# Kernel optimization log

Hardware: AMD Instinct MI355X
Metric: run time of the kernel (lower is better)

The kernel has to match this reference:

```python
import jax, jax.numpy as jnp
import numpy as np

B, H, L, T, V, LAYERS = 512, 256, 256, 64, 128, 2
SOS = 0


def setup_inputs() -> dict:
    key = jax.random.key(0)
    ks = jax.random.split(key, 10)
    s = 0.05
    return {
        "x": jax.random.normal(ks[0], (B, H, 1, L), jnp.float32),          # encoder memory
        "y": jax.random.randint(ks[1], (B, T), 0, V, jnp.int32),            # teacher tokens
        "emb": jax.random.normal(ks[2], (V, H), jnp.float32) * s,           # embedding table
        "attn_w": jax.random.normal(ks[3], (L, 2 * H), jnp.float32) * s,    # attn Linear [out,in]
        "attn_b": jnp.zeros((L,), jnp.float32),
        "comb_w": jax.random.normal(ks[4], (H, 2 * H), jnp.float32) * s,    # attn_combine
        "comb_b": jnp.zeros((H,), jnp.float32),
        "gru_w_ih": jax.random.normal(ks[5], (LAYERS, 3 * H, H), jnp.float32) * s,
        "gru_w_hh": jax.random.normal(ks[6], (LAYERS, 3 * H, H), jnp.float32) * s,
        "gru_b_ih": jnp.zeros((LAYERS, 3 * H), jnp.float32),
        "gru_b_hh": jnp.zeros((LAYERS, 3 * H), jnp.float32),
        "out_w": jax.random.normal(ks[7], (V, H), jnp.float32) * s,
        "out_b": jnp.zeros((V,), jnp.float32),
    }


def reference(x, y, emb, attn_w, attn_b, comb_w, comb_b,
              gru_w_ih, gru_w_hh, gru_b_ih, gru_b_hh, out_w, out_b):
    # x: [B, H, 1, L] -> encoder memory enc: [B, L, H]
    enc = jnp.transpose(x[:, :, 0, :], (0, 2, 1))
    b = x.shape[0]
    h0 = jnp.zeros((LAYERS, b, H), x.dtype)
    # teacher forcing: input at step t is y[:, t-1], with SOS at t=0
    tokens = jnp.concatenate([jnp.full((b, 1), SOS, y.dtype), y[:, :-1]], axis=1)  # [B, T]

    def step(hidden, tok):
        e = emb[tok]  # [B, H] (dropout disabled / eval mode)
        scores = jnp.concatenate([e, hidden[0]], axis=1) @ attn_w.T + attn_b  # [B, L]
        aw = jax.nn.softmax(scores, axis=1)
        applied = jnp.einsum('bl,blh->bh', aw, enc)  # [B, H]
        g = jax.nn.relu(jnp.concatenate([applied, e], axis=1) @ comb_w.T + comb_b)
        xin = g
        hs = []
        for l in range(LAYERS):  # single-step multilayer GRU (PyTorch equations)
            gi = xin @ gru_w_ih[l].T + gru_b_ih[l]
            gh = hidden[l] @ gru_w_hh[l].T + gru_b_hh[l]
            ir, iz, inn = jnp.split(gi, 3, axis=1)
            hr, hz, hn = jnp.split(gh, 3, axis=1)
            r = jax.nn.sigmoid(ir + hr)
            z = jax.nn.sigmoid(iz + hz)
            n = jnp.tanh(inn + r * hn)
            hnew = (1 - z) * n + z * hidden[l]
            hs.append(hnew)
            xin = hnew
        logp = jax.nn.log_softmax(xin @ out_w.T + out_b, axis=1)  # [B, V]
        return jnp.stack(hs), (logp, aw)

    _, (outs, attns) = jax.lax.scan(step, h0, tokens.T)  # outs: [T,B,V], attns: [T,B,L]
    return jnp.transpose(outs, (1, 2, 0)), jnp.transpose(attns, (1, 0, 2))
```

## Files before the change

kernel.cpp:

```cpp
#include <hip/hip_runtime.h>
#include <math.h>

#define B 512
#define H 256
#define L 256
#define T 64
#define V 128
#define LAYERS 2
#define SOS 0

#define OFF_A 0
#define OFF_C 131072
#define OFF_G 262144
#define GRU_LAYER_STRIDE (6 * 65536)
#define GRU_MAT_STRIDE 65536
#define OFF_O (OFF_G + LAYERS * GRU_LAYER_STRIDE)
#define WS_HALVES (OFF_O + 32768)
#define OFF_XT WS_HALVES
#define XT_B_STRIDE (32 * 256 * 8)
#define XT_HALVES ((size_t)B * XT_B_STRIDE)
#define WS_NEED_BYTES ((size_t)(OFF_XT + XT_HALVES) * 2)

typedef _Float16 half8 __attribute__((ext_vector_type(8)));
typedef _Float16 half2t __attribute__((ext_vector_type(2)));
typedef unsigned int u32x4 __attribute__((ext_vector_type(4)));
typedef float f32x4 __attribute__((ext_vector_type(4)));

__device__ __forceinline__ float fdot2(half2t a, half2t b, float c) {
#if __has_builtin(__builtin_amdgcn_fdot2)
    return __builtin_amdgcn_fdot2(a, b, c, false);
#else
    return c + (float)a[0] * (float)b[0] + (float)a[1] * (float)b[1];
#endif
}

union H8 {
    half8 v;
    half2t p[4];
    u32x4 u;
};

__device__ __forceinline__ half8 nt_load_h8(const _Float16* p) {
    H8 t;
    t.u = __builtin_nontemporal_load((const u32x4*)p);
    return t.v;
}

__device__ __forceinline__ float sigmoidf_(float v) {
    return 1.f / (1.f + __expf(-v));
}
__device__ __forceinline__ float fast_tanh(float v) {
    v = fminf(fmaxf(v, -15.f), 15.f);
    float e = __expf(-2.f * v);
    return (1.f - e) / (1.f + e);
}

__global__ void prep_pack(const float* __restrict__ attn_w,
                          const float* __restrict__ comb_w,
                          const float* __restrict__ gru_w_ih,
                          const float* __restrict__ gru_w_hh,
                          const float* __restrict__ out_w,
                          _Float16* __restrict__ ws) {
    int stride = gridDim.x * blockDim.x;
    for (int idx = blockIdx.x * blockDim.x + threadIdx.x; idx < WS_HALVES; idx += stride) {
        float val;
        if (idx < OFF_C) {
            int i = idx & 7, r = idx >> 3;
            int l = r & 255, k8 = r >> 8;
            val = attn_w[l * 512 + k8 * 8 + i];
        } else if (idx < OFF_G) {
            int e = idx - OFF_C;
            int i = e & 7, r = e >> 3;
            int hh = r & 255, k8 = r >> 8;
            val = comb_w[hh * 512 + k8 * 8 + i];
        } else if (idx < OFF_O) {
            int e = idx - OFF_G;
            int layer = e / GRU_LAYER_STRIDE;
            e -= layer * GRU_LAYER_STRIDE;
            int mat = e >> 16;
            e &= 65535;
            int i = e & 7, r = e >> 3;
            int j = r & 255, k8 = r >> 8;
            int k = k8 * 8 + i;
            const float* src = (mat < 3) ? gru_w_ih : gru_w_hh;
            int gate = (mat < 3) ? mat : mat - 3;
            val = src[layer * (768 * 256) + (gate * 256 + j) * 256 + k];
        } else {
            int e = idx - OFF_O;
            int i = e & 7, r = e >> 3;
            int v = r & 127, k8 = r >> 7;
            val = out_w[v * 256 + k8 * 8 + i];
        }
        ws[idx] = (_Float16)val;
    }
}

__global__ void prep_x(const float* __restrict__ x, _Float16* __restrict__ xt) {
    const int b = blockIdx.x;
    const int h = threadIdx.x;
    const float* xr = x + ((size_t)b * H + h) * L;
    _Float16* base = xt + (size_t)b * XT_B_STRIDE + h * 8;
#pragma unroll 4
    for (int k8 = 0; k8 < 32; ++k8) {
        float4 v0 = *(const float4*)(xr + k8 * 8);
        float4 v1 = *(const float4*)(xr + k8 * 8 + 4);
        half8 o;
        o[0] = (_Float16)v0.x; o[1] = (_Float16)v0.y;
        o[2] = (_Float16)v0.z; o[3] = (_Float16)v0.w;
        o[4] = (_Float16)v1.x; o[5] = (_Float16)v1.y;
        o[6] = (_Float16)v1.z; o[7] = (_Float16)v1.w;
        *(half8*)(base + k8 * 2048) = o;
    }
}

template <bool USE_XT>
__global__ __launch_bounds__(512, 2) void decoder_kernel(
    const float* __restrict__ x,
    const int* __restrict__ y,
    const float* __restrict__ emb,
    const float* __restrict__ attn_b,
    const float* __restrict__ comb_b,
    const float* __restrict__ gru_b_ih,
    const float* __restrict__ gru_b_hh,
    const float* __restrict__ out_b,
    const _Float16* __restrict__ wsh,
    const _Float16* __restrict__ xt,
    float* __restrict__ out) {
    __shared__ __align__(16) _Float16 ehf[2][512];
    __shared__ __align__(16) _Float16 hfs[LAYERS][2][256];
    __shared__ __align__(16) float h32[LAYERS][2][256];
    __shared__ __align__(16) _Float16 apf[2][256];
    __shared__ __align__(16) _Float16 gfv[2][256];
    __shared__ __align__(16) _Float16 awf[2][256];
    __shared__ __align__(16) float aw32[2][256];
    __shared__ __align__(16) float pbuf[2][2][3][256];
    __shared__ __align__(16) float po[2][2][128];
    __shared__ __align__(16) float lgbuf[2][128][33];

    const int tid = threadIdx.x;
    const int G = tid >> 8;
    const int h = tid & 255;
    const int lane = tid & 63;
    const int w = tid >> 6;
    const int b0 = blockIdx.x * 2;

    const _Float16* AW = wsh + OFF_A;
    const _Float16* CW = wsh + OFF_C;
    const _Float16* OW = wsh + OFF_O;

    const float ab = attn_b[h];
    const float cb = comb_b[h];
    const float ob = (h < V) ? out_b[h] : 0.f;
    float b_ir[LAYERS], b_iz[LAYERS], b_in[LAYERS], b_hr[LAYERS], b_hz[LAYERS], b_hn[LAYERS];
#pragma unroll
    for (int l = 0; l < LAYERS; ++l) {
        b_ir[l] = gru_b_ih[l * 768 + h];
        b_iz[l] = gru_b_ih[l * 768 + 256 + h];
        b_in[l] = gru_b_ih[l * 768 + 512 + h];
        b_hr[l] = gru_b_hh[l * 768 + h];
        b_hz[l] = gru_b_hh[l * 768 + 256 + h];
        b_hn[l] = gru_b_hh[l * 768 + 512 + h];
    }

#pragma unroll
    for (int l = 0; l < LAYERS; ++l) {
        h32[l][G][h] = 0.f;
        hfs[l][G][h] = (_Float16)0.f;
    }
    ehf[G][256 + h] = (_Float16)0.f;
    __syncthreads();

    for (int t = 0; t < T; ++t) {
        {
            int tok = (t == 0) ? SOS : y[(b0 + G) * T + (t - 1)];
            ehf[G][h] = (_Float16)emb[tok * H + h];
        }
        __syncthreads();

        {
            float a00 = 0.f, a01 = 0.f, a10 = 0.f, a11 = 0.f;
            const _Float16* wp = AW + ((G * 32) << 11) + (h << 3);
            const _Float16* e0 = &ehf[0][G << 8];
            const _Float16* e1 = &ehf[1][G << 8];
#pragma unroll 4
            for (int k8 = 0; k8 < 32; ++k8) {
                H8 uw, u0, u1;
                uw.v = *(const half8*)(wp + (k8 << 11));
                u0.v = *(const half8*)(e0 + (k8 << 3));
                u1.v = *(const half8*)(e1 + (k8 << 3));
                a00 = fdot2(uw.p[0], u0.p[0], a00);
                a00 = fdot2(uw.p[1], u0.p[1], a00);
                a01 = fdot2(uw.p[2], u0.p[2], a01);
                a01 = fdot2(uw.p[3], u0.p[3], a01);
                a10 = fdot2(uw.p[0], u1.p[0], a10);
                a10 = fdot2(uw.p[1], u1.p[1], a10);
                a11 = fdot2(uw.p[2], u1.p[2], a11);
                a11 = fdot2(uw.p[3], u1.p[3], a11);
            }
            float bias = (G == 0) ? ab : 0.f;
            pbuf[G][0][0][h] = a00 + a01 + bias;
            pbuf[G][1][0][h] = a10 + a11 + bias;
        }
        __syncthreads();

        if (w < 2) {
            const int r = w;
            float s0 = pbuf[0][r][0][lane] + pbuf[1][r][0][lane];
            float s1 = pbuf[0][r][0][lane + 64] + pbuf[1][r][0][lane + 64];
            float s2 = pbuf[0][r][0][lane + 128] + pbuf[1][r][0][lane + 128];
            float s3 = pbuf[0][r][0][lane + 192] + pbuf[1][r][0][lane + 192];
            float m = fmaxf(fmaxf(s0, s1), fmaxf(s2, s3));
            for (int off = 32; off; off >>= 1) m = fmaxf(m, __shfl_xor(m, off));
            float e0 = __expf(s0 - m), e1 = __expf(s1 - m);
            float e2 = __expf(s2 - m), e3 = __expf(s3 - m);
            float s = e0 + e1 + e2 + e3;
            for (int off = 32; off; off >>= 1) s += __shfl_xor(s, off);
            float inv = 1.f / s;
            e0 *= inv; e1 *= inv; e2 *= inv; e3 *= inv;
            if (USE_XT) {
                awf[r][lane] = (_Float16)e0;
                awf[r][lane + 64] = (_Float16)e1;
                awf[r][lane + 128] = (_Float16)e2;
                awf[r][lane + 192] = (_Float16)e3;
            } else {
                aw32[r][lane] = e0;
                aw32[r][lane + 64] = e1;
                aw32[r][lane + 128] = e2;
                aw32[r][lane + 192] = e3;
            }
            float* outA = out + (size_t)B * V * T + ((size_t)(b0 + r) * T + t) * L;
            __builtin_nontemporal_store(e0, outA + lane);
            __builtin_nontemporal_store(e1, outA + lane + 64);
            __builtin_nontemporal_store(e2, outA + lane + 128);
            __builtin_nontemporal_store(e3, outA + lane + 192);
        }
        __syncthreads();

        if (USE_XT) {
            const _Float16* xrow = xt + (size_t)(b0 + G) * XT_B_STRIDE + (h << 3);
            const _Float16* ap = &awf[G][0];
            float a0 = 0.f, a1 = 0.f;
#pragma unroll 4
            for (int k8 = 0; k8 < 32; ++k8) {
                H8 uw, ua;
                uw.v = nt_load_h8(xrow + (k8 << 11));
                ua.v = *(const half8*)(ap + (k8 << 3));
                a0 = fdot2(uw.p[0], ua.p[0], a0);
                a0 = fdot2(uw.p[1], ua.p[1], a0);
                a1 = fdot2(uw.p[2], ua.p[2], a1);
                a1 = fdot2(uw.p[3], ua.p[3], a1);
            }
            apf[G][h] = (_Float16)(a0 + a1);
        } else {
            const float* xrow = x + ((size_t)(b0 + G) * H + h) * L;
            float a0 = 0.f, a1 = 0.f;
#pragma unroll 4
            for (int l = 0; l < L; l += 8) {
                float4 x0 = *(const float4*)(xrow + l);
                float4 x1 = *(const float4*)(xrow + l + 4);
                float4 w0 = *(const float4*)&aw32[G][l];
                float4 w1 = *(const float4*)&aw32[G][l + 4];
                a0 += x0.x * w0.x + x0.y * w0.y + x0.z * w0.z + x0.w * w0.w;
                a1 += x1.x * w1.x + x1.y * w1.y + x1.z * w1.z + x1.w * w1.w;
            }
            apf[G][h] = (_Float16)(a0 + a1);
        }
        __syncthreads();

        {
            float a00 = 0.f, a01 = 0.f, a10 = 0.f, a11 = 0.f;
            const _Float16* wp = CW + ((G * 32) << 11) + (h << 3);
            const _Float16* i0 = (G == 0) ? &apf[0][0] : &ehf[0][0];
            const _Float16* i1 = (G == 0) ? &apf[1][0] : &ehf[1][0];
#pragma unroll 4
            for (int k8 = 0; k8 < 32; ++k8) {
                H8 uw, u0, u1;
                uw.v = *(const half8*)(wp + (k8 << 11));
                u0.v = *(const half8*)(i0 + (k8 << 3));
                u1.v = *(const half8*)(i1 + (k8 << 3));
                a00 = fdot2(uw.p[0], u0.p[0], a00);
                a00 = fdot2(uw.p[1], u0.p[1], a00);
                a01 = fdot2(uw.p[2], u0.p[2], a01);
                a01 = fdot2(uw.p[3], u0.p[3], a01);
                a10 = fdot2(uw.p[0], u1.p[0], a10);
                a10 = fdot2(uw.p[1], u1.p[1], a10);
                a11 = fdot2(uw.p[2], u1.p[2], a11);
                a11 = fdot2(uw.p[3], u1.p[3], a11);
            }
            pbuf[G][0][1][h] = a00 + a01;
            pbuf[G][1][1][h] = a10 + a11;
        }
        __syncthreads();
        gfv[G][h] = (_Float16)fmaxf(pbuf[0][G][1][h] + pbuf[1][G][1][h] + cb, 0.f);
        __syncthreads();

#pragma unroll
        for (int layer = 0; layer < LAYERS; ++layer) {
            const _Float16* GW = wsh + OFF_G + layer * GRU_LAYER_STRIDE + G * 3 * GRU_MAT_STRIDE;
            const _Float16* act0;
            const _Float16* act1;
            if (G == 0) {
                act0 = (layer == 0) ? &gfv[0][0] : &hfs[0][0][0];
                act1 = (layer == 0) ? &gfv[1][0] : &hfs[0][1][0];
            } else {
                act0 = &hfs[layer][0][0];
                act1 = &hfs[layer][1][0];
            }
            float aA0 = 0.f, aB0 = 0.f, aC0 = 0.f, aA1 = 0.f, aB1 = 0.f, aC1 = 0.f;
#pragma unroll 4
            for (int k8 = 0; k8 < 32; ++k8) {
                H8 w0, w1, w2, u0, u1;
                const int off = (k8 << 11) + (h << 3);
                w0.v = *(const half8*)(GW + off);
                w1.v = *(const half8*)(GW + GRU_MAT_STRIDE + off);
                w2.v = *(const half8*)(GW + 2 * GRU_MAT_STRIDE + off);
                u0.v = *(const half8*)(act0 + (k8 << 3));
                u1.v = *(const half8*)(act1 + (k8 << 3));
#pragma unroll
                for (int p = 0; p < 4; ++p) {
                    aA0 = fdot2(w0.p[p], u0.p[p], aA0);
                    aB0 = fdot2(w1.p[p], u0.p[p], aB0);
                    aC0 = fdot2(w2.p[p], u0.p[p], aC0);
                    aA1 = fdot2(w0.p[p], u1.p[p], aA1);
                    aB1 = fdot2(w1.p[p], u1.p[p], aB1);
                    aC1 = fdot2(w2.p[p], u1.p[p], aC1);
                }
            }
            pbuf[G][0][0][h] = aA0;
            pbuf[G][0][1][h] = aB0;
            pbuf[G][0][2][h] = aC0;
            pbuf[G][1][0][h] = aA1;
            pbuf[G][1][1][h] = aB1;
            pbuf[G][1][2][h] = aC1;
            __syncthreads();
            {
                float gi_r = pbuf[0][G][0][h], gi_z = pbuf[0][G][1][h], gi_n = pbuf[0][G][2][h];
                float gh_r = pbuf[1][G][0][h], gh_z = pbuf[1][G][1][h], gh_n = pbuf[1][G][2][h];
                float rr = sigmoidf_(gi_r + b_ir[layer] + gh_r + b_hr[layer]);
                float zz = sigmoidf_(gi_z + b_iz[layer] + gh_z + b_hz[layer]);
                float nn = fast_tanh(gi_n + b_in[layer] + rr * (gh_n + b_hn[layer]));
                float hnew = (1.f - zz) * nn + zz * h32[layer][G][h];
                h32[layer][G][h] = hnew;
                hfs[layer][G][h] = (_Float16)hnew;
                if (layer == 0) ehf[G][256 + h] = (_Float16)hnew;
            }
            __syncthreads();
        }

        {
            const int v = h & 127;
            const int kh = h >> 7;
            const _Float16* hp = &hfs[1][G][0] + (kh << 7);
            const _Float16* wp = OW + ((kh * 16) << 10) + (v << 3);
            float a0 = 0.f, a1 = 0.f;
#pragma unroll 4
            for (int k8 = 0; k8 < 16; ++k8) {
                H8 uw, ua;
                uw.v = *(const half8*)(wp + (k8 << 10));
                ua.v = *(const half8*)(hp + (k8 << 3));
                a0 = fdot2(uw.p[0], ua.p[0], a0);
                a0 = fdot2(uw.p[1], ua.p[1], a0);
                a1 = fdot2(uw.p[2], ua.p[2], a1);
                a1 = fdot2(uw.p[3], ua.p[3], a1);
            }
            po[kh][G][v] = a0 + a1 + ((kh == 0) ? ob : 0.f);
        }
        __syncthreads();

        if (w < 2) {
            const int r = w;
            float l0 = po[0][r][lane] + po[1][r][lane];
            float l1 = po[0][r][lane + 64] + po[1][r][lane + 64];
            float m = fmaxf(l0, l1);
            for (int off = 32; off; off >>= 1) m = fmaxf(m, __shfl_xor(m, off));
            float s = __expf(l0 - m) + __expf(l1 - m);
            for (int off = 32; off; off >>= 1) s += __shfl_xor(s, off);
            float lse = m + __logf(s);
            lgbuf[r][lane][t & 31] = l0 - lse;
            lgbuf[r][lane + 64][t & 31] = l1 - lse;
        }

        if ((t & 31) == 31) {
            __syncthreads();
            const int tb = t & ~31;
#pragma unroll
            for (int c = 0; c < 4; ++c) {
                int fidx = c * 512 + tid;
                int r = fidx >> 10;
                int rem = fidx & 1023;
                int v = rem >> 3;
                int tq = (rem & 7) << 2;
                f32x4 vec = {lgbuf[r][v][tq], lgbuf[r][v][tq + 1],
                             lgbuf[r][v][tq + 2], lgbuf[r][v][tq + 3]};
                float* dst = out + (size_t)(b0 + r) * V * T + (size_t)v * T + tb + tq;
                __builtin_nontemporal_store(vec, (f32x4*)dst);
            }
        }
    }
}

extern "C" void kernel_launch(void* const* d_in, const int* in_sizes, int n_in,
                              void* d_out, int out_size, void* d_ws, size_t ws_size,
                              hipStream_t stream) {
    const float* x = (const float*)d_in[0];
    const int* y = (const int*)d_in[1];
    const float* emb = (const float*)d_in[2];
    const float* attn_w = (const float*)d_in[3];
    const float* attn_b = (const float*)d_in[4];
    const float* comb_w = (const float*)d_in[5];
    const float* comb_b = (const float*)d_in[6];
    const float* gru_w_ih = (const float*)d_in[7];
    const float* gru_w_hh = (const float*)d_in[8];
    const float* gru_b_ih = (const float*)d_in[9];
    const float* gru_b_hh = (const float*)d_in[10];
    const float* out_w = (const float*)d_in[11];
    const float* out_b = (const float*)d_in[12];
    float* out = (float*)d_out;
    _Float16* ws = (_Float16*)d_ws;

    prep_pack<<<512, 256, 0, stream>>>(attn_w, comb_w, gru_w_ih, gru_w_hh, out_w, ws);
    if (ws_size >= WS_NEED_BYTES) {
        _Float16* xt = ws + OFF_XT;
        prep_x<<<B, 256, 0, stream>>>(x, xt);
        decoder_kernel<true><<<B / 2, 512, 0, stream>>>(
            x, y, emb, attn_b, comb_b, gru_b_ih, gru_b_hh, out_b, ws, xt, out);
    } else {
        decoder_kernel<false><<<B / 2, 512, 0, stream>>>(
            x, y, emb, attn_b, comb_b, gru_b_ih, gru_b_hh, out_b, ws, nullptr, out);
    }
}
```

Before: 2.025 ms.

## Split K across four thread groups with 1024-thread decoder blocks

Doubles the block size to 1024 threads and splits every matvec (attention scores, attention apply, combine, GRU gates, output projection) along the reduction dimension across four groups. Partial sums go through shared memory and are added before each nonlinearity. This shortens each thread's serial dot-product loop to raise parallelism per batch pair, since the grid has only 256 blocks. In exchange it adds extra shared-memory reductions and barriers per step, and the elementwise phases now leave half the threads idle.

```diff
diff --git a/kernel.cpp b/kernel.cpp
--- a/kernel.cpp
+++ b/kernel.cpp
@@ -114,7 +114,7 @@
 }
 
 template <bool USE_XT>
-__global__ __launch_bounds__(512, 2) void decoder_kernel(
+__global__ __launch_bounds__(1024, 4) void decoder_kernel(
     const float* __restrict__ x,
     const int* __restrict__ y,
     const float* __restrict__ emb,
@@ -133,8 +133,9 @@
     __shared__ __align__(16) _Float16 gfv[2][256];
     __shared__ __align__(16) _Float16 awf[2][256];
     __shared__ __align__(16) float aw32[2][256];
-    __shared__ __align__(16) float pbuf[2][2][3][256];
-    __shared__ __align__(16) float po[2][2][128];
+    __shared__ __align__(16) float pbuf[4][2][256];
+    __shared__ __align__(16) float pgru[4][2][3][256];
+    __shared__ __align__(16) float po[4][2][128];
     __shared__ __align__(16) float lgbuf[2][128][33];
 
     const int tid = threadIdx.x;
@@ -150,7 +151,7 @@
 
     const float ab = attn_b[h];
     const float cb = comb_b[h];
-    const float ob = (h < V) ? out_b[h] : 0.f;
+    const float ob = out_b[h & 127];
     float b_ir[LAYERS], b_iz[LAYERS], b_in[LAYERS], b_hr[LAYERS], b_hz[LAYERS], b_hn[LAYERS];
 #pragma unroll
     for (int l = 0; l < LAYERS; ++l) {
@@ -162,16 +163,18 @@
         b_hn[l] = gru_b_hh[l * 768 + 512 + h];
     }
 
+    if (G < 2) {
 #pragma unroll
-    for (int l = 0; l < LAYERS; ++l) {
-        h32[l][G][h] = 0.f;
-        hfs[l][G][h] = (_Float16)0.f;
-    }
-    ehf[G][256 + h] = (_Float16)0.f;
+        for (int l = 0; l < LAYERS; ++l) {
+            h32[l][G][h] = 0.f;
+            hfs[l][G][h] = (_Float16)0.f;
+        }
+        ehf[G][256 + h] = (_Float16)0.f;
+    }
     __syncthreads();
 
     for (int t = 0; t < T; ++t) {
-        {
+        if (G < 2) {
             int tok = (t == 0) ? SOS : y[(b0 + G) * T + (t - 1)];
             ehf[G][h] = (_Float16)emb[tok * H + h];
         }
@@ -179,11 +182,11 @@
 
         {
             float a00 = 0.f, a01 = 0.f, a10 = 0.f, a11 = 0.f;
-            const _Float16* wp = AW + ((G * 32) << 11) + (h << 3);
-            const _Float16* e0 = &ehf[0][G << 8];
-            const _Float16* e1 = &ehf[1][G << 8];
-#pragma unroll 4
-            for (int k8 = 0; k8 < 32; ++k8) {
+            const _Float16* wp = AW + ((G * 16) << 11) + (h << 3);
+            const _Float16* e0 = &ehf[0][G << 7];
+            const _Float16* e1 = &ehf[1][G << 7];
+#pragma unroll 4
+            for (int k8 = 0; k8 < 16; ++k8) {
                 H8 uw, u0, u1;
                 uw.v = *(const half8*)(wp + (k8 << 11));
                 u0.v = *(const half8*)(e0 + (k8 << 3));
@@ -198,17 +201,17 @@
                 a11 = fdot2(uw.p[3], u1.p[3], a11);
             }
             float bias = (G == 0) ? ab : 0.f;
-            pbuf[G][0][0][h] = a00 + a01 + bias;
-            pbuf[G][1][0][h] = a10 + a11 + bias;
+            pbuf[G][0][h] = a00 + a01 + bias;
+            pbuf[G][1][h] = a10 + a11 + bias;
         }
         __syncthreads();
 
         if (w < 2) {
             const int r = w;
-            float s0 = pbuf[0][r][0][lane] + pbuf[1][r][0][lane];
-            float s1 = pbuf[0][r][0][lane + 64] + pbuf[1][r][0][lane + 64];
-            float s2 = pbuf[0][r][0][lane + 128] + pbuf[1][r][0][lane + 128];
-            float s3 = pbuf[0][r][0][lane + 192] + pbuf[1][r][0][lane + 192];
+            float s0 = pbuf[0][r][lane] + pbuf[1][r][lane] + pbuf[2][r][lane] + pbuf[3][r][lane];
+            float s1 = pbuf[0][r][lane + 64] + pbuf[1][r][lane + 64] + pbuf[2][r][lane + 64] + pbuf[3][r][lane + 64];
+            float s2 = pbuf[0][r][lane + 128] + pbuf[1][r][lane + 128] + pbuf[2][r][lane + 128] + pbuf[3][r][lane + 128];
+            float s3 = pbuf[0][r][lane + 192] + pbuf[1][r][lane + 192] + pbuf[2][r][lane + 192] + pbuf[3][r][lane + 192];
             float m = fmaxf(fmaxf(s0, s1), fmaxf(s2, s3));
             for (int off = 32; off; off >>= 1) m = fmaxf(m, __shfl_xor(m, off));
             float e0 = __expf(s0 - m), e1 = __expf(s1 - m);
@@ -236,44 +239,52 @@
         }
         __syncthreads();
 
-        if (USE_XT) {
-            const _Float16* xrow = xt + (size_t)(b0 + G) * XT_B_STRIDE + (h << 3);
-            const _Float16* ap = &awf[G][0];
-            float a0 = 0.f, a1 = 0.f;
-#pragma unroll 4
-            for (int k8 = 0; k8 < 32; ++k8) {
-                H8 uw, ua;
-                uw.v = nt_load_h8(xrow + (k8 << 11));
-                ua.v = *(const half8*)(ap + (k8 << 3));
-                a0 = fdot2(uw.p[0], ua.p[0], a0);
-                a0 = fdot2(uw.p[1], ua.p[1], a0);
-                a1 = fdot2(uw.p[2], ua.p[2], a1);
-                a1 = fdot2(uw.p[3], ua.p[3], a1);
-            }
-            apf[G][h] = (_Float16)(a0 + a1);
-        } else {
-            const float* xrow = x + ((size_t)(b0 + G) * H + h) * L;
-            float a0 = 0.f, a1 = 0.f;
-#pragma unroll 4
-            for (int l = 0; l < L; l += 8) {
-                float4 x0 = *(const float4*)(xrow + l);
-                float4 x1 = *(const float4*)(xrow + l + 4);
-                float4 w0 = *(const float4*)&aw32[G][l];
-                float4 w1 = *(const float4*)&aw32[G][l + 4];
-                a0 += x0.x * w0.x + x0.y * w0.y + x0.z * w0.z + x0.w * w0.w;
-                a1 += x1.x * w1.x + x1.y * w1.y + x1.z * w1.z + x1.w * w1.w;
-            }
-            apf[G][h] = (_Float16)(a0 + a1);
-        }
+        {
+            const int r = G & 1;
+            const int q = G >> 1;
+            if (USE_XT) {
+                const _Float16* xrow = xt + (size_t)(b0 + r) * XT_B_STRIDE + (q << 15) + (h << 3);
+                const _Float16* ap = &awf[r][q << 7];
+                float a0 = 0.f, a1 = 0.f;
+#pragma unroll 4
+                for (int k8 = 0; k8 < 16; ++k8) {
+                    H8 uw, ua;
+                    uw.v = nt_load_h8(xrow + (k8 << 11));
+                    ua.v = *(const half8*)(ap + (k8 << 3));
+                    a0 = fdot2(uw.p[0], ua.p[0], a0);
+                    a0 = fdot2(uw.p[1], ua.p[1], a0);
+                    a1 = fdot2(uw.p[2], ua.p[2], a1);
+                    a1 = fdot2(uw.p[3], ua.p[3], a1);
+                }
+                pbuf[G][0][h] = a0 + a1;
+            } else {
+                const float* xrow = x + ((size_t)(b0 + r) * H + h) * L + (q << 7);
+                const float* ap = &aw32[r][q << 7];
+                float a0 = 0.f, a1 = 0.f;
+#pragma unroll 4
+                for (int l = 0; l < 128; l += 8) {
+                    float4 x0 = *(const float4*)(xrow + l);
+                    float4 x1 = *(const float4*)(xrow + l + 4);
+                    float4 w0 = *(const float4*)(ap + l);
+                    float4 w1 = *(const float4*)(ap + l + 4);
+                    a0 += x0.x * w0.x + x0.y * w0.y + x0.z * w0.z + x0.w * w0.w;
+                    a1 += x1.x * w1.x + x1.y * w1.y + x1.z * w1.z + x1.w * w1.w;
+                }
+                pbuf[G][0][h] = a0 + a1;
+            }
+        }
+        __syncthreads();
+
+        if (G < 2) apf[G][h] = (_Float16)(pbuf[G][0][h] + pbuf[G + 2][0][h]);
         __syncthreads();
 
         {
             float a00 = 0.f, a01 = 0.f, a10 = 0.f, a11 = 0.f;
-            const _Float16* wp = CW + ((G * 32) << 11) + (h << 3);
-            const _Float16* i0 = (G == 0) ? &apf[0][0] : &ehf[0][0];
-            const _Float16* i1 = (G == 0) ? &apf[1][0] : &ehf[1][0];
-#pragma unroll 4
-            for (int k8 = 0; k8 < 32; ++k8) {
+            const _Float16* wp = CW + ((G * 16) << 11) + (h << 3);
+            const _Float16* i0 = (G < 2) ? &apf[0][G << 7] : &ehf[0][(G - 2) << 7];
+            const _Float16* i1 = (G < 2) ? &apf[1][G << 7] : &ehf[1][(G - 2) << 7];
+#pragma unroll 4
+            for (int k8 = 0; k8 < 16; ++k8) {
                 H8 uw, u0, u1;
                 uw.v = *(const half8*)(wp + (k8 << 11));
                 u0.v = *(const half8*)(i0 + (k8 << 3));
@@ -287,30 +298,35 @@
                 a11 = fdot2(uw.p[2], u1.p[2], a11);
                 a11 = fdot2(uw.p[3], u1.p[3], a11);
             }
-            pbuf[G][0][1][h] = a00 + a01;
-            pbuf[G][1][1][h] = a10 + a11;
-        }
-        __syncthreads();
-        gfv[G][h] = (_Float16)fmaxf(pbuf[0][G][1][h] + pbuf[1][G][1][h] + cb, 0.f);
+            pbuf[G][0][h] = a00 + a01;
+            pbuf[G][1][h] = a10 + a11;
+        }
+        __syncthreads();
+        if (G < 2)
+            gfv[G][h] = (_Float16)fmaxf(
+                pbuf[0][G][h] + pbuf[1][G][h] + pbuf[2][G][h] + pbuf[3][G][h] + cb, 0.f);
         __syncthreads();
 
 #pragma unroll
         for (int layer = 0; layer < LAYERS; ++layer) {
-            const _Float16* GW = wsh + OFF_G + layer * GRU_LAYER_STRIDE + G * 3 * GRU_MAT_STRIDE;
+            const int mh = G >> 1;
+            const int kq = G & 1;
+            const _Float16* GW = wsh + OFF_G + layer * GRU_LAYER_STRIDE +
+                                 mh * 3 * GRU_MAT_STRIDE + ((kq * 16) << 11) + (h << 3);
             const _Float16* act0;
             const _Float16* act1;
-            if (G == 0) {
-                act0 = (layer == 0) ? &gfv[0][0] : &hfs[0][0][0];
-                act1 = (layer == 0) ? &gfv[1][0] : &hfs[0][1][0];
+            if (mh == 0) {
+                act0 = ((layer == 0) ? &gfv[0][0] : &hfs[0][0][0]) + (kq << 7);
+                act1 = ((layer == 0) ? &gfv[1][0] : &hfs[0][1][0]) + (kq << 7);
             } else {
-                act0 = &hfs[layer][0][0];
-                act1 = &hfs[layer][1][0];
+                act0 = &hfs[layer][0][0] + (kq << 7);
+                act1 = &hfs[layer][1][0] + (kq << 7);
             }
             float aA0 = 0.f, aB0 = 0.f, aC0 = 0.f, aA1 = 0.f, aB1 = 0.f, aC1 = 0.f;
 #pragma unroll 4
-            for (int k8 = 0; k8 < 32; ++k8) {
+            for (int k8 = 0; k8 < 16; ++k8) {
                 H8 w0, w1, w2, u0, u1;
-                const int off = (k8 << 11) + (h << 3);
+                const int off = k8 << 11;
                 w0.v = *(const half8*)(GW + off);
                 w1.v = *(const half8*)(GW + GRU_MAT_STRIDE + off);
                 w2.v = *(const half8*)(GW + 2 * GRU_MAT_STRIDE + off);
@@ -326,35 +342,40 @@
                     aC1 = fdot2(w2.p[p], u1.p[p], aC1);
                 }
             }
-            pbuf[G][0][0][h] = aA0;
-            pbuf[G][0][1][h] = aB0;
-            pbuf[G][0][2][h] = aC0;
-            pbuf[G][1][0][h] = aA1;
-            pbuf[G][1][1][h] = aB1;
-            pbuf[G][1][2][h] = aC1;
+            pgru[G][0][0][h] = aA0;
+            pgru[G][0][1][h] = aB0;
+            pgru[G][0][2][h] = aC0;
+            pgru[G][1][0][h] = aA1;
+            pgru[G][1][1][h] = aB1;
+            pgru[G][1][2][h] = aC1;
             __syncthreads();
-            {
-                float gi_r = pbuf[0][G][0][h], gi_z = pbuf[0][G][1][h], gi_n = pbuf[0][G][2][h];
-                float gh_r = pbuf[1][G][0][h], gh_z = pbuf[1][G][1][h], gh_n = pbuf[1][G][2][h];
+            if (G < 2) {
+                const int r = G;
+                float gi_r = pgru[0][r][0][h] + pgru[1][r][0][h];
+                float gi_z = pgru[0][r][1][h] + pgru[1][r][1][h];
+                float gi_n = pgru[0][r][2][h] + pgru[1][r][2][h];
+                float gh_r = pgru[2][r][0][h] + pgru[3][r][0][h];
+                float gh_z = pgru[2][r][1][h] + pgru[3][r][1][h];
+                float gh_n = pgru[2][r][2][h] + pgru[3][r][2][h];
                 float rr = sigmoidf_(gi_r + b_ir[layer] + gh_r + b_hr[layer]);
                 float zz = sigmoidf_(gi_z + b_iz[layer] + gh_z + b_hz[layer]);
                 float nn = fast_tanh(gi_n + b_in[layer] + rr * (gh_n + b_hn[layer]));
-                float hnew = (1.f - zz) * nn + zz * h32[layer][G][h];
-                h32[layer][G][h] = hnew;
-                hfs[layer][G][h] = (_Float16)hnew;
-                if (layer == 0) ehf[G][256 + h] = (_Float16)hnew;
+                float hnew = (1.f - zz) * nn + zz * h32[layer][r][h];
+                h32[layer][r][h] = hnew;
+                hfs[layer][r][h] = (_Float16)hnew;
+                if (layer == 0) ehf[r][256 + h] = (_Float16)hnew;
             }
             __syncthreads();
         }
 
         {
             const int v = h & 127;
-            const int kh = h >> 7;
-            const _Float16* hp = &hfs[1][G][0] + (kh << 7);
-            const _Float16* wp = OW + ((kh * 16) << 10) + (v << 3);
+            const int r = h >> 7;
+            const _Float16* hp = &hfs[1][r][0] + (G << 6);
+            const _Float16* wp = OW + ((G * 8) << 10) + (v << 3);
             float a0 = 0.f, a1 = 0.f;
 #pragma unroll 4
-            for (int k8 = 0; k8 < 16; ++k8) {
+            for (int k8 = 0; k8 < 8; ++k8) {
                 H8 uw, ua;
                 uw.v = *(const half8*)(wp + (k8 << 10));
                 ua.v = *(const half8*)(hp + (k8 << 3));
@@ -363,14 +384,14 @@
                 a1 = fdot2(uw.p[2], ua.p[2], a1);
                 a1 = fdot2(uw.p[3], ua.p[3], a1);
             }
-            po[kh][G][v] = a0 + a1 + ((kh == 0) ? ob : 0.f);
+            po[G][r][v] = a0 + a1 + ((G == 0) ? ob : 0.f);
         }
         __syncthreads();
 
         if (w < 2) {
             const int r = w;
-            float l0 = po[0][r][lane] + po[1][r][lane];
-            float l1 = po[0][r][lane + 64] + po[1][r][lane + 64];
+            float l0 = po[0][r][lane] + po[1][r][lane] + po[2][r][lane] + po[3][r][lane];
+            float l1 = po[0][r][lane + 64] + po[1][r][lane + 64] + po[2][r][lane + 64] + po[3][r][lane + 64];
             float m = fmaxf(l0, l1);
             for (int off = 32; off; off >>= 1) m = fmaxf(m, __shfl_xor(m, off));
             float s = __expf(l0 - m) + __expf(l1 - m);
@@ -384,8 +405,8 @@
             __syncthreads();
             const int tb = t & ~31;
 #pragma unroll
-            for (int c = 0; c < 4; ++c) {
-                int fidx = c * 512 + tid;
+            for (int c = 0; c < 2; ++c) {
+                int fidx = c * 1024 + tid;
                 int r = fidx >> 10;
                 int rem = fidx & 1023;
                 int v = rem >> 3;
@@ -422,10 +443,10 @@
     if (ws_size >= WS_NEED_BYTES) {
         _Float16* xt = ws + OFF_XT;
         prep_x<<<B, 256, 0, stream>>>(x, xt);
-        decoder_kernel<true><<<B / 2, 512, 0, stream>>>(
+        decoder_kernel<true><<<B / 2, 1024, 0, stream>>>(
             x, y, emb, attn_b, comb_b, gru_b_ih, gru_b_hh, out_b, ws, xt, out);
     } else {
-        decoder_kernel<false><<<B / 2, 512, 0, stream>>>(
+        decoder_kernel<false><<<B / 2, 1024, 0, stream>>>(
             x, y, emb, attn_b, comb_b, gru_b_ih, gru_b_hh, out_b, ws, nullptr, out);
     }
 }
```

New measurement: 2.087 ms. +3.1%, slower.

## Precompute embedding projection tables and stage GRU/output weights in registers and LDS

Applied to the files above, without the earlier changes.

Adds a prep kernel that precomputes attn_w·emb and comb_w·emb per vocabulary token, so each step looks up a table entry instead of doing the embedding half of the attention and combine matmuls. This halves the K dimension of those two matmuls. It also keeps part of the GRU weights resident in registers and LDS across all timesteps and moves the output projection weights into LDS, cutting repeated global loads. The logit staging buffer is shrunk to flush every 8 steps. The costs are heavy register and LDS pressure, which may lower occupancy under launch_bounds(512,2), and the tables are rounded to fp16.

```diff
diff --git a/kernel.cpp b/kernel.cpp
--- a/kernel.cpp
+++ b/kernel.cpp
@@ -15,11 +15,16 @@
 #define GRU_LAYER_STRIDE (6 * 65536)
 #define GRU_MAT_STRIDE 65536
 #define OFF_O (OFF_G + LAYERS * GRU_LAYER_STRIDE)
-#define WS_HALVES (OFF_O + 32768)
+#define OFF_SE (OFF_O + 32768)
+#define OFF_CE (OFF_SE + 32768)
+#define WS_HALVES (OFF_CE + 32768)
 #define OFF_XT WS_HALVES
 #define XT_B_STRIDE (32 * 256 * 8)
 #define XT_HALVES ((size_t)B * XT_B_STRIDE)
 #define WS_NEED_BYTES ((size_t)(OFF_XT + XT_HALVES) * 2)
+
+#define PREG 6
+#define KLDS PREG
 
 typedef _Float16 half8 __attribute__((ext_vector_type(8)));
 typedef _Float16 half2t __attribute__((ext_vector_type(2)));
@@ -62,7 +67,7 @@
                           const float* __restrict__ out_w,
                           _Float16* __restrict__ ws) {
     int stride = gridDim.x * blockDim.x;
-    for (int idx = blockIdx.x * blockDim.x + threadIdx.x; idx < WS_HALVES; idx += stride) {
+    for (int idx = blockIdx.x * blockDim.x + threadIdx.x; idx < OFF_SE; idx += stride) {
         float val;
         if (idx < OFF_C) {
             int i = idx & 7, r = idx >> 3;
@@ -95,6 +100,23 @@
     }
 }
 
+__global__ void prep_tabs(const float* __restrict__ attn_w,
+                          const float* __restrict__ comb_w,
+                          const float* __restrict__ emb,
+                          _Float16* __restrict__ ws) {
+    __shared__ float ev[256];
+    const int which = blockIdx.x >> 7;
+    const int v = blockIdx.x & 127;
+    const int l = threadIdx.x;
+    ev[l] = emb[v * 256 + l];
+    __syncthreads();
+    const float* wrow = which ? (comb_w + l * 512 + 256) : (attn_w + l * 512);
+    float s = 0.f;
+#pragma unroll 8
+    for (int k = 0; k < 256; ++k) s += wrow[k] * ev[k];
+    ws[(which ? OFF_CE : OFF_SE) + v * 256 + l] = (_Float16)s;
+}
+
 __global__ void prep_x(const float* __restrict__ x, _Float16* __restrict__ xt) {
     const int b = blockIdx.x;
     const int h = threadIdx.x;
@@ -126,7 +148,6 @@
     const _Float16* __restrict__ wsh,
     const _Float16* __restrict__ xt,
     float* __restrict__ out) {
-    __shared__ __align__(16) _Float16 ehf[2][512];
     __shared__ __align__(16) _Float16 hfs[LAYERS][2][256];
     __shared__ __align__(16) float h32[LAYERS][2][256];
     __shared__ __align__(16) _Float16 apf[2][256];
@@ -135,7 +156,9 @@
     __shared__ __align__(16) float aw32[2][256];
     __shared__ __align__(16) float pbuf[2][2][3][256];
     __shared__ __align__(16) float po[2][2][128];
-    __shared__ __align__(16) float lgbuf[2][128][33];
+    __shared__ __align__(16) float lgbuf[2][128][9];
+    __shared__ __align__(16) _Float16 glds[LAYERS][2][3][2048];
+    __shared__ __align__(16) _Float16 olds[32768];
 
     const int tid = threadIdx.x;
     const int G = tid >> 8;
@@ -146,11 +169,12 @@
 
     const _Float16* AW = wsh + OFF_A;
     const _Float16* CW = wsh + OFF_C;
-    const _Float16* OW = wsh + OFF_O;
+    const _Float16* SE = wsh + OFF_SE;
+    const _Float16* CE = wsh + OFF_CE;
 
     const float ab = attn_b[h];
     const float cb = comb_b[h];
-    const float ob = (h < V) ? out_b[h] : 0.f;
+    const float ob = out_b[h & 127];
     float b_ir[LAYERS], b_iz[LAYERS], b_in[LAYERS], b_hr[LAYERS], b_hz[LAYERS], b_hn[LAYERS];
 #pragma unroll
     for (int l = 0; l < LAYERS; ++l) {
@@ -162,28 +186,44 @@
         b_hn[l] = gru_b_hh[l * 768 + 512 + h];
     }
 
+    H8 wreg[LAYERS][3][PREG];
+#pragma unroll
+    for (int l = 0; l < LAYERS; ++l)
+#pragma unroll
+        for (int m = 0; m < 3; ++m)
+#pragma unroll
+            for (int kp = 0; kp < PREG; ++kp)
+                wreg[l][m][kp].v = *(const half8*)(wsh + OFF_G + l * GRU_LAYER_STRIDE +
+                                                   (G * 3 + m) * GRU_MAT_STRIDE +
+                                                   (kp << 11) + (h << 3));
+
+    for (int idx = tid; idx < LAYERS * 2 * 3 * 2048; idx += 512) {
+        int l = idx / 12288, r1 = idx % 12288;
+        int role = r1 / 6144, r2 = r1 % 6144;
+        int m = r2 / 2048, e = r2 % 2048;
+        glds[l][role][m][e] = wsh[OFF_G + l * GRU_LAYER_STRIDE +
+                                  (role * 3 + m) * GRU_MAT_STRIDE + (KLDS << 11) + e];
+    }
+    for (int idx = tid; idx < 32768; idx += 512) olds[idx] = wsh[OFF_O + idx];
+
 #pragma unroll
     for (int l = 0; l < LAYERS; ++l) {
         h32[l][G][h] = 0.f;
         hfs[l][G][h] = (_Float16)0.f;
     }
-    ehf[G][256 + h] = (_Float16)0.f;
     __syncthreads();
 
     for (int t = 0; t < T; ++t) {
-        {
-            int tok = (t == 0) ? SOS : y[(b0 + G) * T + (t - 1)];
-            ehf[G][h] = (_Float16)emb[tok * H + h];
-        }
-        __syncthreads();
+        const int tok0 = (t == 0) ? SOS : y[b0 * T + (t - 1)];
+        const int tok1 = (t == 0) ? SOS : y[(b0 + 1) * T + (t - 1)];
 
         {
             float a00 = 0.f, a01 = 0.f, a10 = 0.f, a11 = 0.f;
-            const _Float16* wp = AW + ((G * 32) << 11) + (h << 3);
-            const _Float16* e0 = &ehf[0][G << 8];
-            const _Float16* e1 = &ehf[1][G << 8];
+            const _Float16* wp = AW + (((32 + G * 16)) << 11) + (h << 3);
+            const _Float16* e0 = &hfs[0][0][G << 7];
+            const _Float16* e1 = &hfs[0][1][G << 7];
 #pragma unroll 4
-            for (int k8 = 0; k8 < 32; ++k8) {
+            for (int k8 = 0; k8 < 16; ++k8) {
                 H8 uw, u0, u1;
                 uw.v = *(const half8*)(wp + (k8 << 11));
                 u0.v = *(const half8*)(e0 + (k8 << 3));
@@ -197,9 +237,13 @@
                 a11 = fdot2(uw.p[2], u1.p[2], a11);
                 a11 = fdot2(uw.p[3], u1.p[3], a11);
             }
-            float bias = (G == 0) ? ab : 0.f;
-            pbuf[G][0][0][h] = a00 + a01 + bias;
-            pbuf[G][1][0][h] = a10 + a11 + bias;
+            if (G == 0) {
+                pbuf[0][0][0][h] = a00 + a01 + ab + (float)SE[tok0 * 256 + h];
+                pbuf[0][1][0][h] = a10 + a11 + ab + (float)SE[tok1 * 256 + h];
+            } else {
+                pbuf[1][0][0][h] = a00 + a01;
+                pbuf[1][1][0][h] = a10 + a11;
+            }
         }
         __syncthreads();
 
@@ -269,11 +313,11 @@
 
         {
             float a00 = 0.f, a01 = 0.f, a10 = 0.f, a11 = 0.f;
-            const _Float16* wp = CW + ((G * 32) << 11) + (h << 3);
-            const _Float16* i0 = (G == 0) ? &apf[0][0] : &ehf[0][0];
-            const _Float16* i1 = (G == 0) ? &apf[1][0] : &ehf[1][0];
+            const _Float16* wp = CW + ((G * 16) << 11) + (h << 3);
+            const _Float16* i0 = &apf[0][G << 7];
+            const _Float16* i1 = &apf[1][G << 7];
 #pragma unroll 4
-            for (int k8 = 0; k8 < 32; ++k8) {
+            for (int k8 = 0; k8 < 16; ++k8) {
                 H8 uw, u0, u1;
                 uw.v = *(const half8*)(wp + (k8 << 11));
                 u0.v = *(const half8*)(i0 + (k8 << 3));
@@ -291,12 +335,15 @@
             pbuf[G][1][1][h] = a10 + a11;
         }
         __syncthreads();
-        gfv[G][h] = (_Float16)fmaxf(pbuf[0][G][1][h] + pbuf[1][G][1][h] + cb, 0.f);
+        {
+            const int tokg = G ? tok1 : tok0;
+            gfv[G][h] = (_Float16)fmaxf(pbuf[0][G][1][h] + pbuf[1][G][1][h] + cb +
+                                            (float)CE[tokg * 256 + h], 0.f);
+        }
         __syncthreads();
 
 #pragma unroll
         for (int layer = 0; layer < LAYERS; ++layer) {
-            const _Float16* GW = wsh + OFF_G + layer * GRU_LAYER_STRIDE + G * 3 * GRU_MAT_STRIDE;
             const _Float16* act0;
             const _Float16* act1;
             if (G == 0) {
@@ -307,10 +354,44 @@
                 act1 = &hfs[layer][1][0];
             }
             float aA0 = 0.f, aB0 = 0.f, aC0 = 0.f, aA1 = 0.f, aB1 = 0.f, aC1 = 0.f;
-#pragma unroll 4
-            for (int k8 = 0; k8 < 32; ++k8) {
+#pragma unroll
+            for (int kp = 0; kp < PREG; ++kp) {
+                H8 u0, u1;
+                u0.v = *(const half8*)(act0 + (kp << 3));
+                u1.v = *(const half8*)(act1 + (kp << 3));
+#pragma unroll
+                for (int p = 0; p < 4; ++p) {
+                    aA0 = fdot2(wreg[layer][0][kp].p[p], u0.p[p], aA0);
+                    aB0 = fdot2(wreg[layer][1][kp].p[p], u0.p[p], aB0);
+                    aC0 = fdot2(wreg[layer][2][kp].p[p], u0.p[p], aC0);
+                    aA1 = fdot2(wreg[layer][0][kp].p[p], u1.p[p], aA1);
+                    aB1 = fdot2(wreg[layer][1][kp].p[p], u1.p[p], aB1);
+                    aC1 = fdot2(wreg[layer][2][kp].p[p], u1.p[p], aC1);
+                }
+            }
+            {
                 H8 w0, w1, w2, u0, u1;
-                const int off = (k8 << 11) + (h << 3);
+                w0.v = *(const half8*)(&glds[layer][G][0][h << 3]);
+                w1.v = *(const half8*)(&glds[layer][G][1][h << 3]);
+                w2.v = *(const half8*)(&glds[layer][G][2][h << 3]);
+                u0.v = *(const half8*)(act0 + (KLDS << 3));
+                u1.v = *(const half8*)(act1 + (KLDS << 3));
+#pragma unroll
+                for (int p = 0; p < 4; ++p) {
+                    aA0 = fdot2(w0.p[p], u0.p[p], aA0);
+                    aB0 = fdot2(w1.p[p], u0.p[p], aB0);
+                    aC0 = fdot2(w2.p[p], u0.p[p], aC0);
+                    aA1 = fdot2(w0.p[p], u1.p[p], aA1);
+                    aB1 = fdot2(w1.p[p], u1.p[p], aB1);
+                    aC1 = fdot2(w2.p[p], u1.p[p], aC1);
+                }
+            }
+            const _Float16* GW = wsh + OFF_G + layer * GRU_LAYER_STRIDE +
+                                 G * 3 * GRU_MAT_STRIDE + (h << 3);
+#pragma unroll 5
+            for (int k8 = KLDS + 1; k8 < 32; ++k8) {
+                H8 w0, w1, w2, u0, u1;
+                const int off = k8 << 11;
                 w0.v = *(const half8*)(GW + off);
                 w1.v = *(const half8*)(GW + GRU_MAT_STRIDE + off);
                 w2.v = *(const half8*)(GW + 2 * GRU_MAT_STRIDE + off);
@@ -342,7 +423,6 @@
                 float hnew = (1.f - zz) * nn + zz * h32[layer][G][h];
                 h32[layer][G][h] = hnew;
                 hfs[layer][G][h] = (_Float16)hnew;
-                if (layer == 0) ehf[G][256 + h] = (_Float16)hnew;
             }
             __syncthreads();
         }
@@ -351,7 +431,7 @@
             const int v = h & 127;
             const int kh = h >> 7;
             const _Float16* hp = &hfs[1][G][0] + (kh << 7);
-            const _Float16* wp = OW + ((kh * 16) << 10) + (v << 3);
+            const _Float16* wp = olds + ((kh * 16) << 10) + (v << 3);
             float a0 = 0.f, a1 = 0.f;
 #pragma unroll 4
             for (int k8 = 0; k8 < 16; ++k8) {
@@ -376,25 +456,21 @@
             float s = __expf(l0 - m) + __expf(l1 - m);
             for (int off = 32; off; off >>= 1) s += __shfl_xor(s, off);
             float lse = m + __logf(s);
-            lgbuf[r][lane][t & 31] = l0 - lse;
-            lgbuf[r][lane + 64][t & 31] = l1 - lse;
-        }
-
-        if ((t & 31) == 31) {
+            lgbuf[r][lane][t & 7] = l0 - lse;
+            lgbuf[r][lane + 64][t & 7] = l1 - lse;
+        }
+
+        if ((t & 7) == 7) {
             __syncthreads();
-            const int tb = t & ~31;
-#pragma unroll
-            for (int c = 0; c < 4; ++c) {
-                int fidx = c * 512 + tid;
-                int r = fidx >> 10;
-                int rem = fidx & 1023;
-                int v = rem >> 3;
-                int tq = (rem & 7) << 2;
-                f32x4 vec = {lgbuf[r][v][tq], lgbuf[r][v][tq + 1],
-                             lgbuf[r][v][tq + 2], lgbuf[r][v][tq + 3]};
-                float* dst = out + (size_t)(b0 + r) * V * T + (size_t)v * T + tb + tq;
-                __builtin_nontemporal_store(vec, (f32x4*)dst);
-            }
+            const int tb = t & ~7;
+            int r = tid >> 8;
+            int rem = tid & 255;
+            int v = rem >> 1;
+            int tq = (rem & 1) << 2;
+            f32x4 vec = {lgbuf[r][v][tq], lgbuf[r][v][tq + 1],
+                         lgbuf[r][v][tq + 2], lgbuf[r][v][tq + 3]};
+            float* dst = out + (size_t)(b0 + r) * V * T + (size_t)v * T + tb + tq;
+            __builtin_nontemporal_store(vec, (f32x4*)dst);
         }
     }
 }
@@ -419,6 +495,7 @@
     _Float16* ws = (_Float16*)d_ws;
 
     prep_pack<<<512, 256, 0, stream>>>(attn_w, comb_w, gru_w_ih, gru_w_hh, out_w, ws);
+    prep_tabs<<<256, 256, 0, stream>>>(attn_w, comb_w, emb, ws);
     if (ws_size >= WS_NEED_BYTES) {
         _Float16* xt = ws + OFF_XT;
         prep_x<<<B, 256, 0, stream>>>(x, xt);
```

Result: slower. 2.571 ms (+27.0%).
